# Kernel optimization log

Measured on AMD Instinct MI355X. Metric: run time of the kernel, lower is better.

The kernel has to match this reference:

```python
import jax, jax.numpy as jnp
import numpy as np


def setup_inputs() -> dict:
    key = jax.random.key(0)
    ks = jax.random.split(key, 8)
    B, Q, K, F, FV, C = 8, 2048, 2048, 512, 512, 2
    q = jax.random.normal(ks[0], (B, Q, F), dtype=jnp.float32)
    k = jax.random.normal(ks[1], (B, K, F), dtype=jnp.float32)
    v = jax.random.normal(ks[2], (B, K, FV), dtype=jnp.float32)
    coords_q = jax.random.uniform(ks[3], (B, Q, C), dtype=jnp.float32)
    coords_k = jax.random.uniform(ks[4], (B, K, C), dtype=jnp.float32)
    attn_mask = jax.random.randint(ks[5], (B, Q, K), 0, 2).astype(bool)
    alibi_mask = jax.random.randint(ks[6], (B, Q, K), 0, 2).astype(bool)
    bias_scale = jax.random.uniform(ks[7], (1,), dtype=jnp.float32)
    return {"q": q, "k": k, "v": v, "coords_q": coords_q, "coords_k": coords_k,
            "attn_mask": attn_mask, "alibi_mask": alibi_mask, "bias_scale": bias_scale}


def reference(q, k, v, coords_q, coords_k, attn_mask, alibi_mask, bias_scale):
    # scaled dot-product logits: [B, Q, K]
    scale = k.shape[-1] ** -0.5
    weight_logits = jnp.einsum('bqf,bkf->bqk', q, k) * scale
    # pairwise Euclidean coordinate distances: [B, Q, K]
    diff = coords_q[:, :, None, :] - coords_k[:, None, :, :]
    distances = jnp.linalg.norm(diff, axis=-1)
    # _RunningMeanScaler in eval mode divides by running_mean == 1 (identity)
    scaled_distances = distances * bias_scale  # bias_scale broadcasts from [1]
    scaled_distances = jnp.where(alibi_mask, 0.0, scaled_distances)
    weights = jax.nn.softmax(weight_logits, axis=-1)
    # post-softmax bias subtraction + masking (non-standard attention)
    weights = jnp.where(attn_mask, 0.0, weights - scaled_distances)
    attention = jnp.einsum('bqk,bkf->bqf', weights, v)
    return attention
```

## Files before the change

### kernel.cpp

```cpp
#include <hip/hip_runtime.h>
#include <hip/hip_bf16.h>
#include <math.h>

#define BN  8
#define QN  2048
#define KN  2048
#define FN  512
#define FVN 512

typedef __bf16 bf16x8 __attribute__((ext_vector_type(8)));
typedef __bf16 bf16x4v __attribute__((ext_vector_type(4)));
typedef float  f32x4  __attribute__((ext_vector_type(4)));

__device__ inline bf16x8 pack8(float4 a, float4 b) {
  bf16x8 r;
  r[0] = (__bf16)a.x; r[1] = (__bf16)a.y; r[2] = (__bf16)a.z; r[3] = (__bf16)a.w;
  r[4] = (__bf16)b.x; r[5] = (__bf16)b.y; r[6] = (__bf16)b.z; r[7] = (__bf16)b.w;
  return r;
}

__device__ __forceinline__ void g2l16(const __bf16* g, __bf16* l) {
  __builtin_amdgcn_global_load_lds(
      (const __attribute__((address_space(1))) void*)g,
      (__attribute__((address_space(3))) void*)l,
      16, 0, 0);
}

__global__ __launch_bounds__(256) void prep(
    const float* __restrict__ qm, const float* __restrict__ km,
    const float* __restrict__ vm,
    __bf16* __restrict__ qb, __bf16* __restrict__ kb, __bf16* __restrict__ Vt) {
  const int tid = threadIdx.x;
  if (blockIdx.y == 0) {
    const size_t idx = ((size_t)blockIdx.x * 256 + tid) * 8;
    const float scale = 0.044194173824159216f;
    float4 a = *(const float4*)(qm + idx);
    float4 b = *(const float4*)(qm + idx + 4);
    a.x *= scale; a.y *= scale; a.z *= scale; a.w *= scale;
    b.x *= scale; b.y *= scale; b.z *= scale; b.w *= scale;
    *(bf16x8*)(qb + idx) = pack8(a, b);
  } else if (blockIdx.y == 1) {
    const size_t idx = ((size_t)blockIdx.x * 256 + tid) * 8;
    float4 a = *(const float4*)(km + idx);
    float4 b = *(const float4*)(km + idx + 4);
    *(bf16x8*)(kb + idx) = pack8(a, b);
  } else {
    const int bx = blockIdx.x;
    if (bx >= (KN / 64) * (FVN / 64) * BN) return;
    const int b  = bx >> 8;
    const int f0 = ((bx >> 5) & 7) * 64;
    const int k0 = (bx & 31) * 64;
    __shared__ float tile[64][65];
    const int r = tid >> 4;
    const int c = (tid & 15) * 4;
#pragma unroll
    for (int i = 0; i < 4; i++) {
      float4 u = *(const float4*)(vm + ((size_t)b * KN + k0 + r + i * 16) * FVN + f0 + c);
      tile[r + i * 16][c] = u.x; tile[r + i * 16][c + 1] = u.y;
      tile[r + i * 16][c + 2] = u.z; tile[r + i * 16][c + 3] = u.w;
    }
    __syncthreads();
#pragma unroll
    for (int i = 0; i < 4; i++) {
      int fv = r + i * 16;
      bf16x4v w;
      w[0] = (__bf16)tile[c][fv];     w[1] = (__bf16)tile[c + 1][fv];
      w[2] = (__bf16)tile[c + 2][fv]; w[3] = (__bf16)tile[c + 3][fv];
      *(bf16x4v*)(Vt + ((size_t)b * FVN + f0 + fv) * KN + k0 + c) = w;
    }
  }
}

__global__ __launch_bounds__(256) void gemm_s(
    const __bf16* __restrict__ qb, const __bf16* __restrict__ kb,
    __bf16* __restrict__ Sws, int b0, int q0, int qchunk) {
  __shared__ __align__(16) __bf16 As[2][128][32];
  __shared__ __align__(16) __bf16 Bs[2][128][32];
  const int tid = threadIdx.x;
  const int lane = tid & 63, wave = tid >> 6;
  const int wq = (wave & 1) * 64, wk = (wave >> 1) * 64;
  const int qt = blockIdx.x * 128, kt = blockIdx.y * 128;
  const int z = blockIdx.z, b = b0 + z;
  __bf16* S = Sws + (size_t)z * qchunk * KN;
  const __bf16* Ab = qb + ((size_t)b * QN + q0 + qt) * FN;
  const __bf16* Bb = kb + ((size_t)b * KN + kt) * FN;
  const int srow = lane >> 2;
  const int scol = (lane & 3) * 8;
  const int r = lane & 15, quad = lane >> 4;
  f32x4 acc[4][4] = {};
  for (int f0 = 0; f0 < FN; f0 += 64) {
    __syncthreads();
#pragma unroll
    for (int h = 0; h < 2; h++) {
      const int co = f0 + h * 32 + scol;
      g2l16(Ab + (size_t)(wave * 32 + srow) * FN + co,      &As[h][wave * 32][0]);
      g2l16(Ab + (size_t)(wave * 32 + 16 + srow) * FN + co, &As[h][wave * 32 + 16][0]);
      g2l16(Bb + (size_t)(wave * 32 + srow) * FN + co,      &Bs[h][wave * 32][0]);
      g2l16(Bb + (size_t)(wave * 32 + 16 + srow) * FN + co, &Bs[h][wave * 32 + 16][0]);
    }
    __syncthreads();
#pragma unroll
    for (int h = 0; h < 2; h++) {
      bf16x8 af[4], bf[4];
#pragma unroll
      for (int i = 0; i < 4; i++) af[i] = *(bf16x8*)&As[h][wq + i * 16 + r][quad * 8];
#pragma unroll
      for (int j = 0; j < 4; j++) bf[j] = *(bf16x8*)&Bs[h][wk + j * 16 + r][quad * 8];
#pragma unroll
      for (int i = 0; i < 4; i++)
#pragma unroll
        for (int j = 0; j < 4; j++)
          acc[i][j] = __builtin_amdgcn_mfma_f32_16x16x32_bf16(af[i], bf[j], acc[i][j], 0, 0, 0);
    }
  }
#pragma unroll
  for (int i = 0; i < 4; i++)
#pragma unroll
    for (int j = 0; j < 4; j++)
#pragma unroll
      for (int t = 0; t < 4; t++) {
        int qq = qt + wq + i * 16 + quad * 4 + t;
        int kk = kt + wk + j * 16 + r;
        S[(size_t)qq * KN + kk] = (__bf16)acc[i][j][t];
      }
}

__global__ __launch_bounds__(256) void softmax_w(
    __bf16* __restrict__ Sws,
    const float* __restrict__ cq, const float* __restrict__ ck,
    const int* __restrict__ attn, const int* __restrict__ alibi,
    const float* __restrict__ bsp, int b0, int q0, int qchunk) {
  const int z = blockIdx.z, b = b0 + z;
  const int lane = threadIdx.x & 63, wave = threadIdx.x >> 6;
  const int ql = blockIdx.x * 4 + wave;
  const int qg = q0 + ql;
  __bf16* Srow = Sws + ((size_t)z * qchunk + ql) * KN;
  const int* arow = attn + ((size_t)b * QN + qg) * KN;
  const int* lrow = alibi + ((size_t)b * QN + qg) * KN;
  const float* ckb = ck + (size_t)b * KN * 2;
  bf16x8 s8[4];
#pragma unroll
  for (int c = 0; c < 4; c++) s8[c] = *(bf16x8*)(Srow + c * 512 + lane * 8);
  float p[32];
  float sum = 0.f;
#pragma unroll
  for (int c = 0; c < 4; c++)
#pragma unroll
    for (int i = 0; i < 8; i++) { p[c * 8 + i] = __expf((float)s8[c][i]); sum += p[c * 8 + i]; }
  for (int o = 32; o > 0; o >>= 1) sum += __shfl_xor(sum, o);
  const float inv = 1.0f / sum;
  const float qx = cq[((size_t)b * QN + qg) * 2 + 0];
  const float qy = cq[((size_t)b * QN + qg) * 2 + 1];
  const float bs = bsp[0];
#pragma unroll
  for (int c = 0; c < 4; c++) {
    const int k0 = c * 512 + lane * 8;
    int4 am0 = *(const int4*)(arow + k0);
    int4 am1 = *(const int4*)(arow + k0 + 4);
    int4 al0 = *(const int4*)(lrow + k0);
    int4 al1 = *(const int4*)(lrow + k0 + 4);
    float4 c0 = *(const float4*)(ckb + (size_t)k0 * 2);
    float4 c1 = *(const float4*)(ckb + (size_t)k0 * 2 + 4);
    float4 c2 = *(const float4*)(ckb + (size_t)k0 * 2 + 8);
    float4 c3 = *(const float4*)(ckb + (size_t)k0 * 2 + 12);
    int   am[8] = {am0.x, am0.y, am0.z, am0.w, am1.x, am1.y, am1.z, am1.w};
    int   al[8] = {al0.x, al0.y, al0.z, al0.w, al1.x, al1.y, al1.z, al1.w};
    float kx[8] = {c0.x, c0.z, c1.x, c1.z, c2.x, c2.z, c3.x, c3.z};
    float ky[8] = {c0.y, c0.w, c1.y, c1.w, c2.y, c2.w, c3.y, c3.w};
    bf16x8 w8;
#pragma unroll
    for (int j = 0; j < 8; j++) {
      float dx = qx - kx[j], dy = qy - ky[j];
      float sd = al[j] ? 0.f : sqrtf(dx * dx + dy * dy) * bs;
      float w = am[j] ? 0.f : (p[c * 8 + j] * inv - sd);
      w8[j] = (__bf16)w;
    }
    *(bf16x8*)(Srow + k0) = w8;
  }
}

__global__ __launch_bounds__(256) void gemm_w(
    const __bf16* __restrict__ W, const __bf16* __restrict__ Vt,
    float* __restrict__ out, int b0, int q0, int qchunk) {
  __shared__ __align__(16) __bf16 As[2][128][32];
  __shared__ __align__(16) __bf16 Bs[2][128][32];
  const int tid = threadIdx.x;
  const int lane = tid & 63, wave = tid >> 6;
  const int wq = (wave & 1) * 64, wf = (wave >> 1) * 64;
  const int qt = blockIdx.x * 128, ft = blockIdx.y * 128;
  const int z = blockIdx.z, b = b0 + z;
  const __bf16* Ab = W + ((size_t)z * qchunk + qt) * KN;
  const __bf16* Bb = Vt + ((size_t)b * FVN + ft) * KN;
  const int srow = lane >> 2;
  const int scol = (lane & 3) * 8;
  const int r = lane & 15, quad = lane >> 4;
  f32x4 acc[4][4] = {};
  for (int k0 = 0; k0 < KN; k0 += 64) {
    __syncthreads();
#pragma unroll
    for (int h = 0; h < 2; h++) {
      const int co = k0 + h * 32 + scol;
      g2l16(Ab + (size_t)(wave * 32 + srow) * KN + co,      &As[h][wave * 32][0]);
      g2l16(Ab + (size_t)(wave * 32 + 16 + srow) * KN + co, &As[h][wave * 32 + 16][0]);
      g2l16(Bb + (size_t)(wave * 32 + srow) * KN + co,      &Bs[h][wave * 32][0]);
      g2l16(Bb + (size_t)(wave * 32 + 16 + srow) * KN + co, &Bs[h][wave * 32 + 16][0]);
    }
    __syncthreads();
#pragma unroll
    for (int h = 0; h < 2; h++) {
      bf16x8 af[4], bf[4];
#pragma unroll
      for (int i = 0; i < 4; i++) af[i] = *(bf16x8*)&As[h][wq + i * 16 + r][quad * 8];
#pragma unroll
      for (int j = 0; j < 4; j++) bf[j] = *(bf16x8*)&Bs[h][wf + j * 16 + r][quad * 8];
#pragma unroll
      for (int i = 0; i < 4; i++)
#pragma unroll
        for (int j = 0; j < 4; j++)
          acc[i][j] = __builtin_amdgcn_mfma_f32_16x16x32_bf16(af[i], bf[j], acc[i][j], 0, 0, 0);
    }
  }
#pragma unroll
  for (int i = 0; i < 4; i++)
#pragma unroll
    for (int j = 0; j < 4; j++)
#pragma unroll
      for (int t = 0; t < 4; t++) {
        int qq = q0 + qt + wq + i * 16 + quad * 4 + t;
        int fv = ft + wf + j * 16 + r;
        out[((size_t)b * QN + qq) * FVN + fv] = acc[i][j][t];
      }
}

extern "C" void kernel_launch(void* const* d_in, const int* in_sizes, int n_in,
                              void* d_out, int out_size, void* d_ws, size_t ws_size,
                              hipStream_t stream) {
  (void)in_sizes; (void)n_in; (void)out_size;
  const float* qm   = (const float*)d_in[0];
  const float* km   = (const float*)d_in[1];
  const float* vm   = (const float*)d_in[2];
  const float* cq   = (const float*)d_in[3];
  const float* ck   = (const float*)d_in[4];
  const int*   attn = (const int*)d_in[5];
  const int*   alibi= (const int*)d_in[6];
  const float* bsp  = (const float*)d_in[7];
  float* out = (float*)d_out;

  __bf16* qb  = (__bf16*)d_ws;
  __bf16* kb  = qb + (size_t)BN * QN * FN;
  __bf16* Vt  = kb + (size_t)BN * KN * FN;
  __bf16* Sws = Vt + (size_t)BN * FVN * KN;
  const size_t fixed = ((size_t)BN * QN * FN + (size_t)BN * KN * FN +
                        (size_t)BN * FVN * KN) * 2;
  int nb = BN, qc = QN;
  while (nb > 1 && fixed + (size_t)nb * qc * KN * 2 > ws_size) nb >>= 1;
  while (qc > 128 && fixed + (size_t)nb * qc * KN * 2 > ws_size) qc >>= 1;

  prep<<<dim3((BN * QN * FN) / 2048, 3), 256, 0, stream>>>(qm, km, vm, qb, kb, Vt);
  for (int b0 = 0; b0 < BN; b0 += nb) {
    for (int q0 = 0; q0 < QN; q0 += qc) {
      gemm_s<<<dim3(qc / 128, KN / 128, nb), 256, 0, stream>>>(qb, kb, Sws, b0, q0, qc);
      softmax_w<<<dim3(qc / 4, 1, nb), 256, 0, stream>>>(Sws, cq, ck, attn, alibi, bsp, b0, q0, qc);
      gemm_w<<<dim3(qc / 128, FVN / 128, nb), 256, 0, stream>>>(Sws, Vt, out, b0, q0, qc);
    }
  }
}
```

Measured before the change: 464.4 us.

## Fuse softmax row sums into QK GEMM and masking into PV GEMM

The first GEMM's epilogue now computes exp of each bf16 logit and atomically accumulates per-row sums into a small buffer, which a memset clears before each chunk. The separate softmax kernel is removed, and a new PV GEMM recomputes exp, normalization, distance bias and masks on the fly while loading the weight tile. This drops one full read and write of the S matrix and one kernel launch. In exchange the new GEMM uses 64-row tiles with the whole FV width per block, gives up the double-buffered LDS layout, syncs twice per 32-wide k step and reads masks per tile, so occupancy and overlap may be lower.

```diff
diff --git a/kernel.cpp b/kernel.cpp
--- a/kernel.cpp
+++ b/kernel.cpp
@@ -73,7 +73,8 @@
 
 __global__ __launch_bounds__(256) void gemm_s(
     const __bf16* __restrict__ qb, const __bf16* __restrict__ kb,
-    __bf16* __restrict__ Sws, int b0, int q0, int qchunk) {
+    __bf16* __restrict__ Sws, float* __restrict__ sums,
+    int b0, int q0, int qchunk) {
   __shared__ __align__(16) __bf16 As[2][128][32];
   __shared__ __align__(16) __bf16 Bs[2][128][32];
   const int tid = threadIdx.x;
@@ -116,53 +117,59 @@
 #pragma unroll
   for (int i = 0; i < 4; i++)
 #pragma unroll
-    for (int j = 0; j < 4; j++)
-#pragma unroll
-      for (int t = 0; t < 4; t++) {
-        int qq = qt + wq + i * 16 + quad * 4 + t;
-        int kk = kt + wk + j * 16 + r;
-        S[(size_t)qq * KN + kk] = (__bf16)acc[i][j][t];
+    for (int t = 0; t < 4; t++) {
+      float e = 0.f;
+#pragma unroll
+      for (int j = 0; j < 4; j++) {
+        __bf16 sb = (__bf16)acc[i][j][t];
+        S[(size_t)(qt + wq + i * 16 + quad * 4 + t) * KN + (kt + wk + j * 16 + r)] = sb;
+        e += __expf((float)sb);
       }
-}
-
-__global__ __launch_bounds__(256) void softmax_w(
-    __bf16* __restrict__ Sws,
+      e += __shfl_xor(e, 1); e += __shfl_xor(e, 2);
+      e += __shfl_xor(e, 4); e += __shfl_xor(e, 8);
+      if (r == 0)
+        atomicAdd(&sums[(size_t)z * qchunk + qt + wq + i * 16 + quad * 4 + t], e);
+    }
+}
+
+__global__ __launch_bounds__(256) void gemm_wv(
+    const __bf16* __restrict__ S, const float* __restrict__ sums,
+    const __bf16* __restrict__ Vt,
     const float* __restrict__ cq, const float* __restrict__ ck,
     const int* __restrict__ attn, const int* __restrict__ alibi,
-    const float* __restrict__ bsp, int b0, int q0, int qchunk) {
+    const float* __restrict__ bsp, float* __restrict__ out,
+    int b0, int q0, int qchunk) {
+  __shared__ __align__(16) __bf16 Ws[64][32];
+  __shared__ __align__(16) __bf16 Vs[512][32];
+  const int tid = threadIdx.x;
+  const int lane = tid & 63, wave = tid >> 6;
+  const int qt = blockIdx.x * 64;
   const int z = blockIdx.z, b = b0 + z;
-  const int lane = threadIdx.x & 63, wave = threadIdx.x >> 6;
-  const int ql = blockIdx.x * 4 + wave;
-  const int qg = q0 + ql;
-  __bf16* Srow = Sws + ((size_t)z * qchunk + ql) * KN;
+  const int wr = tid >> 2;
+  const int wc = (tid & 3) * 8;
+  const int qg = q0 + qt + wr;
+  const float qx = cq[((size_t)b * QN + qg) * 2 + 0];
+  const float qy = cq[((size_t)b * QN + qg) * 2 + 1];
+  const float inv = 1.0f / sums[(size_t)z * qchunk + qt + wr];
+  const float bs = bsp[0];
+  const __bf16* Srow = S + ((size_t)z * qchunk + qt + wr) * KN;
   const int* arow = attn + ((size_t)b * QN + qg) * KN;
   const int* lrow = alibi + ((size_t)b * QN + qg) * KN;
   const float* ckb = ck + (size_t)b * KN * 2;
-  bf16x8 s8[4];
-#pragma unroll
-  for (int c = 0; c < 4; c++) s8[c] = *(bf16x8*)(Srow + c * 512 + lane * 8);
-  float p[32];
-  float sum = 0.f;
-#pragma unroll
-  for (int c = 0; c < 4; c++)
-#pragma unroll
-    for (int i = 0; i < 8; i++) { p[c * 8 + i] = __expf((float)s8[c][i]); sum += p[c * 8 + i]; }
-  for (int o = 32; o > 0; o >>= 1) sum += __shfl_xor(sum, o);
-  const float inv = 1.0f / sum;
-  const float qx = cq[((size_t)b * QN + qg) * 2 + 0];
-  const float qy = cq[((size_t)b * QN + qg) * 2 + 1];
-  const float bs = bsp[0];
-#pragma unroll
-  for (int c = 0; c < 4; c++) {
-    const int k0 = c * 512 + lane * 8;
-    int4 am0 = *(const int4*)(arow + k0);
-    int4 am1 = *(const int4*)(arow + k0 + 4);
-    int4 al0 = *(const int4*)(lrow + k0);
-    int4 al1 = *(const int4*)(lrow + k0 + 4);
-    float4 c0 = *(const float4*)(ckb + (size_t)k0 * 2);
-    float4 c1 = *(const float4*)(ckb + (size_t)k0 * 2 + 4);
-    float4 c2 = *(const float4*)(ckb + (size_t)k0 * 2 + 8);
-    float4 c3 = *(const float4*)(ckb + (size_t)k0 * 2 + 12);
+  const __bf16* Vb = Vt + ((size_t)b * FVN + wave * 128) * KN;
+  const int srow = lane >> 2, scol = (lane & 3) * 8;
+  const int r = lane & 15, quad = lane >> 4;
+  f32x4 acc[4][8] = {};
+  for (int k0 = 0; k0 < KN; k0 += 32) {
+    bf16x8 s8 = *(const bf16x8*)(Srow + k0 + wc);
+    int4 am0 = *(const int4*)(arow + k0 + wc);
+    int4 am1 = *(const int4*)(arow + k0 + wc + 4);
+    int4 al0 = *(const int4*)(lrow + k0 + wc);
+    int4 al1 = *(const int4*)(lrow + k0 + wc + 4);
+    float4 c0 = *(const float4*)(ckb + (size_t)(k0 + wc) * 2);
+    float4 c1 = *(const float4*)(ckb + (size_t)(k0 + wc) * 2 + 4);
+    float4 c2 = *(const float4*)(ckb + (size_t)(k0 + wc) * 2 + 8);
+    float4 c3 = *(const float4*)(ckb + (size_t)(k0 + wc) * 2 + 12);
     int   am[8] = {am0.x, am0.y, am0.z, am0.w, am1.x, am1.y, am1.z, am1.w};
     int   al[8] = {al0.x, al0.y, al0.z, al0.w, al1.x, al1.y, al1.z, al1.w};
     float kx[8] = {c0.x, c0.z, c1.x, c1.z, c2.x, c2.z, c3.x, c3.z};
@@ -172,62 +179,34 @@
     for (int j = 0; j < 8; j++) {
       float dx = qx - kx[j], dy = qy - ky[j];
       float sd = al[j] ? 0.f : sqrtf(dx * dx + dy * dy) * bs;
-      float w = am[j] ? 0.f : (p[c * 8 + j] * inv - sd);
+      float w = am[j] ? 0.f : (__expf((float)s8[j]) * inv - sd);
       w8[j] = (__bf16)w;
     }
-    *(bf16x8*)(Srow + k0) = w8;
-  }
-}
-
-__global__ __launch_bounds__(256) void gemm_w(
-    const __bf16* __restrict__ W, const __bf16* __restrict__ Vt,
-    float* __restrict__ out, int b0, int q0, int qchunk) {
-  __shared__ __align__(16) __bf16 As[2][128][32];
-  __shared__ __align__(16) __bf16 Bs[2][128][32];
-  const int tid = threadIdx.x;
-  const int lane = tid & 63, wave = tid >> 6;
-  const int wq = (wave & 1) * 64, wf = (wave >> 1) * 64;
-  const int qt = blockIdx.x * 128, ft = blockIdx.y * 128;
-  const int z = blockIdx.z, b = b0 + z;
-  const __bf16* Ab = W + ((size_t)z * qchunk + qt) * KN;
-  const __bf16* Bb = Vt + ((size_t)b * FVN + ft) * KN;
-  const int srow = lane >> 2;
-  const int scol = (lane & 3) * 8;
-  const int r = lane & 15, quad = lane >> 4;
-  f32x4 acc[4][4] = {};
-  for (int k0 = 0; k0 < KN; k0 += 64) {
-    __syncthreads();
-#pragma unroll
-    for (int h = 0; h < 2; h++) {
-      const int co = k0 + h * 32 + scol;
-      g2l16(Ab + (size_t)(wave * 32 + srow) * KN + co,      &As[h][wave * 32][0]);
-      g2l16(Ab + (size_t)(wave * 32 + 16 + srow) * KN + co, &As[h][wave * 32 + 16][0]);
-      g2l16(Bb + (size_t)(wave * 32 + srow) * KN + co,      &Bs[h][wave * 32][0]);
-      g2l16(Bb + (size_t)(wave * 32 + 16 + srow) * KN + co, &Bs[h][wave * 32 + 16][0]);
-    }
-    __syncthreads();
-#pragma unroll
-    for (int h = 0; h < 2; h++) {
-      bf16x8 af[4], bf[4];
-#pragma unroll
-      for (int i = 0; i < 4; i++) af[i] = *(bf16x8*)&As[h][wq + i * 16 + r][quad * 8];
-#pragma unroll
-      for (int j = 0; j < 4; j++) bf[j] = *(bf16x8*)&Bs[h][wf + j * 16 + r][quad * 8];
+    __syncthreads();
+    *(bf16x8*)&Ws[wr][wc] = w8;
+#pragma unroll
+    for (int h = 0; h < 8; h++)
+      g2l16(Vb + (size_t)(h * 16 + srow) * KN + k0 + scol, &Vs[wave * 128 + h * 16][0]);
+    __syncthreads();
+    bf16x8 af[4];
+#pragma unroll
+    for (int i = 0; i < 4; i++) af[i] = *(bf16x8*)&Ws[i * 16 + r][quad * 8];
+#pragma unroll
+    for (int j = 0; j < 8; j++) {
+      bf16x8 bfv = *(bf16x8*)&Vs[wave * 128 + j * 16 + r][quad * 8];
 #pragma unroll
       for (int i = 0; i < 4; i++)
-#pragma unroll
-        for (int j = 0; j < 4; j++)
-          acc[i][j] = __builtin_amdgcn_mfma_f32_16x16x32_bf16(af[i], bf[j], acc[i][j], 0, 0, 0);
+        acc[i][j] = __builtin_amdgcn_mfma_f32_16x16x32_bf16(af[i], bfv, acc[i][j], 0, 0, 0);
     }
   }
 #pragma unroll
   for (int i = 0; i < 4; i++)
 #pragma unroll
-    for (int j = 0; j < 4; j++)
+    for (int j = 0; j < 8; j++)
 #pragma unroll
       for (int t = 0; t < 4; t++) {
-        int qq = q0 + qt + wq + i * 16 + quad * 4 + t;
-        int fv = ft + wf + j * 16 + r;
+        int qq = q0 + qt + i * 16 + quad * 4 + t;
+        int fv = wave * 128 + j * 16 + r;
         out[((size_t)b * QN + qq) * FVN + fv] = acc[i][j][t];
       }
 }
@@ -249,19 +228,21 @@
   __bf16* qb  = (__bf16*)d_ws;
   __bf16* kb  = qb + (size_t)BN * QN * FN;
   __bf16* Vt  = kb + (size_t)BN * KN * FN;
-  __bf16* Sws = Vt + (size_t)BN * FVN * KN;
   const size_t fixed = ((size_t)BN * QN * FN + (size_t)BN * KN * FN +
                         (size_t)BN * FVN * KN) * 2;
   int nb = BN, qc = QN;
-  while (nb > 1 && fixed + (size_t)nb * qc * KN * 2 > ws_size) nb >>= 1;
-  while (qc > 128 && fixed + (size_t)nb * qc * KN * 2 > ws_size) qc >>= 1;
+  while (nb > 1 && fixed + (size_t)nb * qc * (KN * 2 + 4) > ws_size) nb >>= 1;
+  while (qc > 128 && fixed + (size_t)nb * qc * (KN * 2 + 4) > ws_size) qc >>= 1;
+  __bf16* Sws  = Vt + (size_t)BN * FVN * KN;
+  float*  sums = (float*)((char*)Sws + (size_t)nb * qc * KN * 2);
 
   prep<<<dim3((BN * QN * FN) / 2048, 3), 256, 0, stream>>>(qm, km, vm, qb, kb, Vt);
   for (int b0 = 0; b0 < BN; b0 += nb) {
     for (int q0 = 0; q0 < QN; q0 += qc) {
-      gemm_s<<<dim3(qc / 128, KN / 128, nb), 256, 0, stream>>>(qb, kb, Sws, b0, q0, qc);
-      softmax_w<<<dim3(qc / 4, 1, nb), 256, 0, stream>>>(Sws, cq, ck, attn, alibi, bsp, b0, q0, qc);
-      gemm_w<<<dim3(qc / 128, FVN / 128, nb), 256, 0, stream>>>(Sws, Vt, out, b0, q0, qc);
-    }
-  }
-}
+      hipMemsetAsync(sums, 0, (size_t)nb * qc * 4, stream);
+      gemm_s<<<dim3(qc / 128, KN / 128, nb), 256, 0, stream>>>(qb, kb, Sws, sums, b0, q0, qc);
+      gemm_wv<<<dim3(qc / 64, 1, nb), 256, 0, stream>>>(Sws, sums, Vt, cq, ck,
+                                                        attn, alibi, bsp, out, b0, q0, qc);
+    }
+  }
+}
```

New measurement: 535.5 us. 1.15x slower.
